# Kernel optimization log

Hardware: AMD Instinct MI355X
Metric: run time of the kernel (lower is better)

The kernel has to match this reference:

```python
import jax, jax.numpy as jnp
import numpy as np

NEG_SLOPE = 0.2
EPS = 1e-16


def setup_inputs() -> dict:
    key = jax.random.key(0)
    k1, k2, k3, k4 = jax.random.split(key, 4)
    N, H, F, E = 50000, 4, 32, 800000
    nodes_features = jax.random.normal(k1, (N, H, F), dtype=jnp.float32)
    edge_index = jax.random.randint(k2, (2, E), 0, N, dtype=jnp.int64)
    scoring_fn_source = jax.random.normal(k3, (1, H, F), dtype=jnp.float32)
    scoring_fn_target = jax.random.normal(k4, (1, H, F), dtype=jnp.float32)
    return {
        "nodes_features": nodes_features,
        "scoring_fn_source": scoring_fn_source,
        "scoring_fn_target": scoring_fn_target,
        "edge_index": edge_index,
    }


def reference(nodes_features, scoring_fn_source, scoring_fn_target, edge_index):
    # nodes_features: [N, H, F]; edge_index: [2, E] with row 0 = target, row 1 = source
    num_of_nodes = nodes_features.shape[0]
    trg = edge_index[0]
    src = edge_index[1]

    # Per-node attention logits per head: [N, H]
    scores_source = (nodes_features * scoring_fn_source).sum(axis=-1)
    scores_target = (nodes_features * scoring_fn_target).sum(axis=-1)

    # Lift N -> E via gather: [E, H]
    scores_lifted = scores_source[src] + scores_target[trg]
    src_nodes_features_lifted = nodes_features[src]  # [E, H, F]

    scores_per_edge = jax.nn.leaky_relu(scores_lifted, NEG_SLOPE)
    # Global max subtraction for numerical stability (matches original code)
    scores_per_edge = scores_per_edge - scores_per_edge.max()
    exp_scores = jnp.exp(scores_per_edge)

    # Segment softmax denominator via scatter-add, then gather back per edge
    neighborhood_sums = jax.ops.segment_sum(exp_scores, trg, num_segments=num_of_nodes)
    denom = neighborhood_sums[trg]  # [E, H]

    attentions_per_edge = (exp_scores / (denom + EPS))[..., None]  # [E, H, 1]
    return attentions_per_edge, src_nodes_features_lifted
```

## Files before the change

### kernel.cpp

```cpp
#include <hip/hip_runtime.h>

#define NEG_SLOPE 0.2f
#define EPSV 1e-16f
#define NBMAX 256
#define BSHIFT 8

typedef float f32x4 __attribute__((ext_vector_type(4)));
typedef float f32x2 __attribute__((ext_vector_type(2)));
typedef short s16x2 __attribute__((ext_vector_type(2)));
typedef unsigned u32x2 __attribute__((ext_vector_type(2)));

__device__ __forceinline__ unsigned fenc(float f) {
    unsigned b = __float_as_uint(f);
    return b ^ ((b & 0x80000000u) ? 0xFFFFFFFFu : 0x80000000u);
}
__device__ __forceinline__ float fdec(unsigned u) {
    unsigned b = (u & 0x80000000u) ? (u ^ 0x80000000u) : ~u;
    return __uint_as_float(b);
}
#define FENC_NEG_INF 0x007FFFFFu

__device__ __forceinline__ unsigned f32_to_bf16_rne(float f) {
    unsigned u = __float_as_uint(f);
    unsigned lsb = (u >> 16) & 1u;
    return (u + 0x7FFFu + lsb) >> 16;
}

__device__ __forceinline__ void pk_atomic_add_bf16(unsigned* addr, float a, float b) {
#if __has_builtin(__builtin_amdgcn_global_atomic_fadd_v2bf16)
    s16x2 v;
    v.x = (short)f32_to_bf16_rne(a);
    v.y = (short)f32_to_bf16_rne(b);
    typedef __attribute__((address_space(1))) s16x2 gs16x2;
    __builtin_amdgcn_global_atomic_fadd_v2bf16((gs16x2*)(void*)addr, v);
#else
    unsigned old = *addr, assumed;
    do {
        assumed = old;
        float lo = __uint_as_float((assumed & 0xFFFFu) << 16) + a;
        float hi = __uint_as_float(assumed & 0xFFFF0000u) + b;
        unsigned nv = (f32_to_bf16_rne(hi) << 16) | (f32_to_bf16_rne(lo) & 0xFFFFu);
        old = atomicCAS(addr, assumed, nv);
    } while (old != assumed);
#endif
}

__global__ void detect_idx_kernel(const unsigned* __restrict__ ei32,
                                  int* __restrict__ flag,
                                  unsigned* __restrict__ bhist) {
    __shared__ int anynz;
    if (threadIdx.x == 0) anynz = 0;
    __syncthreads();
    unsigned v = ei32[2 * threadIdx.x + 1];
    if (v != 0u) anynz = 1;
    if (threadIdx.x < NBMAX) bhist[threadIdx.x] = 0u;
    __syncthreads();
    if (threadIdx.x == 0) *flag = (anynz ? 0 : 1);
}

__device__ __forceinline__ int load_idx(const void* ei, int is64, size_t k) {
    if (is64) return (int)__builtin_nontemporal_load(&((const long long*)ei)[k]);
    return __builtin_nontemporal_load(&((const int*)ei)[k]);
}

__global__ void node_scores_kernel(const float* __restrict__ nf,
                                   const float* __restrict__ sfs,
                                   const float* __restrict__ sft,
                                   float* __restrict__ ss,
                                   float* __restrict__ st,
                                   unsigned* __restrict__ nsum_zero,
                                   unsigned* __restrict__ gmax,
                                   int NH, int nzero) {
    int i = blockIdx.x * blockDim.x + threadIdx.x;
    if (i >= NH) return;
    if (i == 0) *gmax = FENC_NEG_INF;
    for (int k = i; k < nzero; k += NH) nsum_zero[k] = 0u;
    int h = i & 3;
    const float4* __restrict__ row = (const float4*)(nf + (size_t)i * 32);
    const float4* __restrict__ as  = (const float4*)(sfs + h * 32);
    const float4* __restrict__ at  = (const float4*)(sft + h * 32);
    float accs = 0.f, acct = 0.f;
#pragma unroll
    for (int q = 0; q < 8; ++q) {
        float4 v = row[q];
        float4 a = as[q];
        float4 b = at[q];
        accs += v.x * a.x + v.y * a.y + v.z * a.z + v.w * a.w;
        acct += v.x * b.x + v.y * b.y + v.z * b.z + v.w * b.w;
    }
    ss[i] = accs;
    st[i] = acct;
}

__global__ void bin_hist_kernel(const void* __restrict__ ei,
                                const int* __restrict__ flag,
                                unsigned* __restrict__ bhist, int E) {
    __shared__ unsigned lh[NBMAX];
    for (int i = threadIdx.x; i < NBMAX; i += blockDim.x) lh[i] = 0u;
    __syncthreads();
    int is64 = *flag;
    int per = (E + gridDim.x - 1) / gridDim.x;
    int s = blockIdx.x * per;
    int en = s + per < E ? s + per : E;
    for (int e = s + threadIdx.x; e < en; e += blockDim.x) {
        int src = load_idx(ei, is64, (size_t)E + e);
        atomicAdd(&lh[src >> BSHIFT], 1u);
    }
    __syncthreads();
    for (int i = threadIdx.x; i < NBMAX; i += blockDim.x)
        if (lh[i]) atomicAdd(&bhist[i], lh[i]);
}

__global__ void bin_scan_kernel(const unsigned* __restrict__ bhist,
                                unsigned* __restrict__ bstart,
                                unsigned* __restrict__ bcursor, int nb) {
    if (threadIdx.x == 0) {
        unsigned acc = 0;
        for (int c = 0; c < nb; ++c) {
            bstart[c] = acc;
            bcursor[c] = acc;
            acc += bhist[c];
        }
        bstart[nb] = acc;
    }
}

__global__ void bin_scatter_kernel(const void* __restrict__ ei,
                                   const int* __restrict__ flag,
                                   unsigned* __restrict__ bcursor,
                                   int* __restrict__ perm,
                                   int* __restrict__ ssrc, int E) {
    __shared__ unsigned lh[NBMAX], lbase[NBMAX], lcur[NBMAX];
    for (int i = threadIdx.x; i < NBMAX; i += blockDim.x) { lh[i] = 0u; lcur[i] = 0u; }
    __syncthreads();
    int is64 = *flag;
    int per = (E + gridDim.x - 1) / gridDim.x;
    int s = blockIdx.x * per;
    int en = s + per < E ? s + per : E;
    for (int e = s + threadIdx.x; e < en; e += blockDim.x) {
        int src = load_idx(ei, is64, (size_t)E + e);
        atomicAdd(&lh[src >> BSHIFT], 1u);
    }
    __syncthreads();
    for (int i = threadIdx.x; i < NBMAX; i += blockDim.x)
        lbase[i] = lh[i] ? atomicAdd(&bcursor[i], lh[i]) : 0u;
    __syncthreads();
    for (int e = s + threadIdx.x; e < en; e += blockDim.x) {
        int src = load_idx(ei, is64, (size_t)E + e);
        int b = src >> BSHIFT;
        unsigned pos = lbase[b] + atomicAdd(&lcur[b], 1u);
        perm[pos] = e;
        ssrc[pos] = src;
    }
}

__global__ void edge_exp_sum_pk_kernel(const void* __restrict__ ei,
                                       const int* __restrict__ flag,
                                       const float* __restrict__ ss,
                                       const float* __restrict__ st,
                                       float* __restrict__ pbuf,
                                       unsigned* __restrict__ nsum_pk,
                                       unsigned* __restrict__ gmax,
                                       int E) {
    __shared__ float red[256];
    int is64 = *flag;
    int n2 = E * 2;
    int stride = gridDim.x * blockDim.x;
    float lmax = -__builtin_inff();
    for (int i = blockIdx.x * blockDim.x + threadIdx.x; i < n2; i += stride) {
        int e = i >> 1, hp = i & 1;
        int trg = load_idx(ei, is64, e);
        int src = load_idx(ei, is64, (size_t)E + e);
        f32x2 a = *(const f32x2*)(ss + (size_t)src * 4 + hp * 2);
        f32x2 b = *(const f32x2*)(st + (size_t)trg * 4 + hp * 2);
        float s0 = a.x + b.x, s1 = a.y + b.y;
        float lr0 = s0 > 0.f ? s0 : NEG_SLOPE * s0;
        float lr1 = s1 > 0.f ? s1 : NEG_SLOPE * s1;
        lmax = fmaxf(lmax, fmaxf(lr0, lr1));
        float p0 = __expf(lr0), p1 = __expf(lr1);
        f32x2 pv; pv.x = p0; pv.y = p1;
        __builtin_nontemporal_store(pv, (f32x2*)(pbuf + (size_t)e * 4 + hp * 2));
        pk_atomic_add_bf16(nsum_pk + (size_t)trg * 2 + hp, p0, p1);
    }
    red[threadIdx.x] = lmax;
    __syncthreads();
    for (int off = 128; off > 0; off >>= 1) {
        if (threadIdx.x < off)
            red[threadIdx.x] = fmaxf(red[threadIdx.x], red[threadIdx.x + off]);
        __syncthreads();
    }
    if (threadIdx.x == 0) atomicMax(gmax, fenc(red[0]));
}

__global__ void att_pk_kernel(const void* __restrict__ ei,
                              const int* __restrict__ flag,
                              const float* __restrict__ pbuf,
                              const unsigned* __restrict__ nsum_pk,
                              const unsigned* __restrict__ gmax,
                              float* __restrict__ out,
                              int E) {
    int is64 = *flag;
    float de = EPSV * __expf(fdec(*gmax));
    int stride = gridDim.x * blockDim.x;
    for (int e = blockIdx.x * blockDim.x + threadIdx.x; e < E; e += stride) {
        int trg = load_idx(ei, is64, e);
        u32x2 u = *(const u32x2*)(nsum_pk + (size_t)trg * 2);
        f32x4 d;
        d.x = __uint_as_float((u.x & 0xFFFFu) << 16);
        d.y = __uint_as_float(u.x & 0xFFFF0000u);
        d.z = __uint_as_float((u.y & 0xFFFFu) << 16);
        d.w = __uint_as_float(u.y & 0xFFFF0000u);
        f32x4 p = __builtin_nontemporal_load((const f32x4*)(pbuf + (size_t)e * 4));
        f32x4 a = p / (d + de);
        __builtin_nontemporal_store(a, (f32x4*)(out + (size_t)e * 4));
    }
}

__global__ void gather_sorted_kernel(const unsigned* __restrict__ bstart,
                                     const int* __restrict__ perm,
                                     const int* __restrict__ ssrc,
                                     const f32x4* __restrict__ nf4,
                                     f32x4* __restrict__ out4, int nb) {
    int xcd = blockIdx.x & 7;
    int lb = blockIdx.x >> 3;
    int lstride = (gridDim.x >> 3) * blockDim.x;
    for (int c = xcd; c < nb; c += 8) {
        int js = (int)bstart[c];
        int n = ((int)bstart[c + 1] - js) << 5;
        for (int t = lb * blockDim.x + threadIdx.x; t < n; t += lstride) {
            int j = js + (t >> 5), q = t & 31;
            int e = perm[j];
            int src = ssrc[j];
            f32x4 v = nf4[(size_t)src * 32 + q];
            __builtin_nontemporal_store(v, &out4[(size_t)e * 32 + q]);
        }
    }
}

__global__ void gather_feat_kernel(const void* __restrict__ ei,
                                   const int* __restrict__ flag,
                                   const f32x4* __restrict__ nf4,
                                   f32x4* __restrict__ out4, int E) {
    int is64 = *flag;
    int n = E * 32;
    int stride = gridDim.x * blockDim.x;
    for (int t = blockIdx.x * blockDim.x + threadIdx.x; t < n; t += stride) {
        int e = t >> 5, q = t & 31;
        int src = load_idx(ei, is64, (size_t)E + e);
        f32x4 v = nf4[(size_t)src * 32 + q];
        __builtin_nontemporal_store(v, &out4[(size_t)e * 32 + q]);
    }
}

__device__ __forceinline__ float edge_lr_rc(const void* ei, int is64,
                                            const float* ss, const float* st,
                                            int E, int e, int h, int* trg_out) {
    int trg = load_idx(ei, is64, e);
    int src = load_idx(ei, is64, (size_t)E + e);
    if (trg_out) *trg_out = trg;
    float s = ss[src * 4 + h] + st[trg * 4 + h];
    return s > 0.f ? s : NEG_SLOPE * s;
}

__global__ void zero_fb_kernel(float* __restrict__ nsum, int n) {
    int i = blockIdx.x * blockDim.x + threadIdx.x;
    if (i < n) nsum[i] = 0.f;
}

__global__ void edge_exp_sum_fb_kernel(const void* __restrict__ ei,
                                       const int* __restrict__ flag,
                                       const float* __restrict__ ss,
                                       const float* __restrict__ st,
                                       float* __restrict__ nsum,
                                       unsigned* __restrict__ gmax, int E) {
    __shared__ float red[256];
    int is64 = *flag;
    int n4 = E * 4;
    int stride = gridDim.x * blockDim.x;
    float lmax = -__builtin_inff();
    for (int i = blockIdx.x * blockDim.x + threadIdx.x; i < n4; i += stride) {
        int trg;
        float lr = edge_lr_rc(ei, is64, ss, st, E, i >> 2, i & 3, &trg);
        lmax = fmaxf(lmax, lr);
        atomicAdd(&nsum[trg * 4 + (i & 3)], __expf(lr));
    }
    red[threadIdx.x] = lmax;
    __syncthreads();
    for (int off = 128; off > 0; off >>= 1) {
        if (threadIdx.x < off)
            red[threadIdx.x] = fmaxf(red[threadIdx.x], red[threadIdx.x + off]);
        __syncthreads();
    }
    if (threadIdx.x == 0) atomicMax(gmax, fenc(red[0]));
}

__global__ void att_fb_kernel(const void* __restrict__ ei,
                              const int* __restrict__ flag,
                              const float* __restrict__ ss,
                              const float* __restrict__ st,
                              const unsigned* __restrict__ gmax,
                              const float* __restrict__ nsum,
                              float* __restrict__ out, int E) {
    int i = blockIdx.x * blockDim.x + threadIdx.x;
    if (i >= E * 4) return;
    int is64 = *flag;
    float de = EPSV * __expf(fdec(*gmax));
    int trg;
    float lr = edge_lr_rc(ei, is64, ss, st, E, i >> 2, i & 3, &trg);
    float a = __expf(lr) / (nsum[trg * 4 + (i & 3)] + de);
    __builtin_nontemporal_store(a, &out[i]);
}

extern "C" void kernel_launch(void* const* d_in, const int* in_sizes, int n_in,
                              void* d_out, int out_size, void* d_ws, size_t ws_size,
                              hipStream_t stream) {
    const float* nf  = (const float*)d_in[0];
    const float* sfs = (const float*)d_in[1];
    const float* sft = (const float*)d_in[2];
    const void*  ei  = d_in[3];

    const int NH = in_sizes[0] / 32;
    const int N  = NH / 4;
    const int E  = in_sizes[3] / 2;
    const int nb = (N + (1 << BSHIFT) - 1) >> BSHIFT;

    float* out = (float*)d_out;
    float* ws  = (float*)d_ws;

    float*    ss      = ws;
    float*    st      = ws + NH;
    int*      flag    = (int*)(ws + 2 * (size_t)NH);
    unsigned* gmax    = (unsigned*)(flag + 1);
    float*    pbuf    = ws + 2 * (size_t)NH + 4;
    unsigned* nsum_pk = (unsigned*)(pbuf + (size_t)E * 4);
    unsigned* bhist   = nsum_pk + (size_t)N * 2;
    unsigned* bstart  = bhist + NBMAX;
    unsigned* bcursor = bstart + NBMAX + 1;
    int*      perm    = (int*)(bcursor + NBMAX);
    int*      ssrc    = perm + E;

    size_t need_r9   = ((size_t)2 * NH + 4 + (size_t)E * 4 + (size_t)N * 2) * 4;
    size_t need_sort = need_r9 + ((size_t)3 * NBMAX + 1 + (size_t)E * 2) * 4;
    bool lean = ws_size >= need_r9;
    bool srt  = ws_size >= need_sort;

    const int B = 256;

    detect_idx_kernel<<<1, 256, 0, stream>>>((const unsigned*)ei, flag, bhist);

    if (lean) {
        node_scores_kernel<<<(NH + B - 1) / B, B, 0, stream>>>(
            nf, sfs, sft, ss, st, nsum_pk, gmax, NH, N * 2);
        if (srt) {
            bin_hist_kernel<<<256, B, 0, stream>>>(ei, flag, bhist, E);
            bin_scan_kernel<<<1, 64, 0, stream>>>(bhist, bstart, bcursor, nb);
            bin_scatter_kernel<<<256, B, 0, stream>>>(ei, flag, bcursor, perm, ssrc, E);
        }
        edge_exp_sum_pk_kernel<<<2048, B, 0, stream>>>(ei, flag, ss, st, pbuf,
                                                       nsum_pk, gmax, E);
        att_pk_kernel<<<2048, B, 0, stream>>>(ei, flag, pbuf, nsum_pk, gmax,
                                              out, E);
        if (srt) {
            gather_sorted_kernel<<<4096, B, 0, stream>>>(
                bstart, perm, ssrc, (const f32x4*)nf,
                (f32x4*)(out + (size_t)E * 4), nb);
        } else {
            gather_feat_kernel<<<4096, B, 0, stream>>>(
                ei, flag, (const f32x4*)nf, (f32x4*)(out + (size_t)E * 4), E);
        }
    } else {
        float* nsum_fb = (float*)(gmax + 1);
        node_scores_kernel<<<(NH + B - 1) / B, B, 0, stream>>>(
            nf, sfs, sft, ss, st, (unsigned*)nsum_fb, gmax, NH, 0);
        zero_fb_kernel<<<(NH + B - 1) / B, B, 0, stream>>>(nsum_fb, NH);
        edge_exp_sum_fb_kernel<<<2048, B, 0, stream>>>(ei, flag, ss, st,
                                                       nsum_fb, gmax, E);
        att_fb_kernel<<<(E * 4 + B - 1) / B, B, 0, stream>>>(ei, flag, ss, st,
                                                             gmax, nsum_fb, out, E);
        gather_feat_kernel<<<4096, B, 0, stream>>>(
            ei, flag, (const f32x4*)nf, (f32x4*)(out + (size_t)E * 4), E);
    }
}
```

Measured before the change: 219.9 us.

## Fuse edge exp/sum pass into bin scatter and pack perm/src pairs

Merges the edge score, exp, segment-sum atomics and max reduction into the bin scatter kernel, so the edge index is read once for both the sort and the softmax numerator. The permutation and source arrays are interleaved into one int2 array, so the gather reads one 8-byte record per edge slot. This drops one kernel launch and one full pass over edge_index, but the fused kernel runs only 512 blocks doing heavier per-edge work (including two packed bf16 atomics), which may cut parallelism for the atomic-heavy part.

```diff
diff --git a/kernel.cpp b/kernel.cpp
--- a/kernel.cpp
+++ b/kernel.cpp
@@ -9,6 +9,7 @@
 typedef float f32x2 __attribute__((ext_vector_type(2)));
 typedef short s16x2 __attribute__((ext_vector_type(2)));
 typedef unsigned u32x2 __attribute__((ext_vector_type(2)));
+typedef int i32x2 __attribute__((ext_vector_type(2)));
 
 __device__ __forceinline__ unsigned fenc(float f) {
     unsigned b = __float_as_uint(f);
@@ -125,18 +126,25 @@
     }
 }
 
-__global__ void bin_scatter_kernel(const void* __restrict__ ei,
+__global__ void scatter_exp_kernel(const void* __restrict__ ei,
                                    const int* __restrict__ flag,
+                                   const float* __restrict__ ss,
+                                   const float* __restrict__ st,
+                                   float* __restrict__ pbuf,
+                                   unsigned* __restrict__ nsum_pk,
+                                   unsigned* __restrict__ gmax,
                                    unsigned* __restrict__ bcursor,
-                                   int* __restrict__ perm,
-                                   int* __restrict__ ssrc, int E) {
+                                   i32x2* __restrict__ pe,
+                                   int E) {
     __shared__ unsigned lh[NBMAX], lbase[NBMAX], lcur[NBMAX];
+    __shared__ float red[256];
     for (int i = threadIdx.x; i < NBMAX; i += blockDim.x) { lh[i] = 0u; lcur[i] = 0u; }
     __syncthreads();
     int is64 = *flag;
     int per = (E + gridDim.x - 1) / gridDim.x;
     int s = blockIdx.x * per;
     int en = s + per < E ? s + per : E;
+
     for (int e = s + threadIdx.x; e < en; e += blockDim.x) {
         int src = load_idx(ei, is64, (size_t)E + e);
         atomicAdd(&lh[src >> BSHIFT], 1u);
@@ -145,12 +153,81 @@
     for (int i = threadIdx.x; i < NBMAX; i += blockDim.x)
         lbase[i] = lh[i] ? atomicAdd(&bcursor[i], lh[i]) : 0u;
     __syncthreads();
+
+    float lmax = -__builtin_inff();
     for (int e = s + threadIdx.x; e < en; e += blockDim.x) {
+        int trg = load_idx(ei, is64, e);
         int src = load_idx(ei, is64, (size_t)E + e);
         int b = src >> BSHIFT;
         unsigned pos = lbase[b] + atomicAdd(&lcur[b], 1u);
-        perm[pos] = e;
-        ssrc[pos] = src;
+        i32x2 pr; pr.x = e; pr.y = src;
+        pe[pos] = pr;
+
+        f32x4 a = *(const f32x4*)(ss + (size_t)src * 4);
+        f32x4 bb = *(const f32x4*)(st + (size_t)trg * 4);
+        f32x4 p;
+#pragma unroll
+        for (int h = 0; h < 4; ++h) {
+            float sc = a[h] + bb[h];
+            float lr = sc > 0.f ? sc : NEG_SLOPE * sc;
+            lmax = fmaxf(lmax, lr);
+            p[h] = __expf(lr);
+        }
+        __builtin_nontemporal_store(p, (f32x4*)(pbuf + (size_t)e * 4));
+        pk_atomic_add_bf16(nsum_pk + (size_t)trg * 2 + 0, p[0], p[1]);
+        pk_atomic_add_bf16(nsum_pk + (size_t)trg * 2 + 1, p[2], p[3]);
+    }
+
+    red[threadIdx.x] = lmax;
+    __syncthreads();
+    for (int off = 128; off > 0; off >>= 1) {
+        if (threadIdx.x < off)
+            red[threadIdx.x] = fmaxf(red[threadIdx.x], red[threadIdx.x + off]);
+        __syncthreads();
+    }
+    if (threadIdx.x == 0) atomicMax(gmax, fenc(red[0]));
+}
+
+__global__ void att_pk_kernel(const void* __restrict__ ei,
+                              const int* __restrict__ flag,
+                              const float* __restrict__ pbuf,
+                              const unsigned* __restrict__ nsum_pk,
+                              const unsigned* __restrict__ gmax,
+                              float* __restrict__ out,
+                              int E) {
+    int is64 = *flag;
+    float de = EPSV * __expf(fdec(*gmax));
+    int stride = gridDim.x * blockDim.x;
+    for (int e = blockIdx.x * blockDim.x + threadIdx.x; e < E; e += stride) {
+        int trg = load_idx(ei, is64, e);
+        u32x2 u = *(const u32x2*)(nsum_pk + (size_t)trg * 2);
+        f32x4 d;
+        d.x = __uint_as_float((u.x & 0xFFFFu) << 16);
+        d.y = __uint_as_float(u.x & 0xFFFF0000u);
+        d.z = __uint_as_float((u.y & 0xFFFFu) << 16);
+        d.w = __uint_as_float(u.y & 0xFFFF0000u);
+        f32x4 p = __builtin_nontemporal_load((const f32x4*)(pbuf + (size_t)e * 4));
+        f32x4 a = p / (d + de);
+        __builtin_nontemporal_store(a, (f32x4*)(out + (size_t)e * 4));
+    }
+}
+
+__global__ void gather_sorted_kernel(const unsigned* __restrict__ bstart,
+                                     const i32x2* __restrict__ pe,
+                                     const f32x4* __restrict__ nf4,
+                                     f32x4* __restrict__ out4, int nb) {
+    int xcd = blockIdx.x & 7;
+    int lb = blockIdx.x >> 3;
+    int lstride = (gridDim.x >> 3) * blockDim.x;
+    for (int c = xcd; c < nb; c += 8) {
+        int js = (int)bstart[c];
+        int n = ((int)bstart[c + 1] - js) << 5;
+        for (int t = lb * blockDim.x + threadIdx.x; t < n; t += lstride) {
+            int j = js + (t >> 5), q = t & 31;
+            i32x2 pr = pe[j];
+            f32x4 v = nf4[(size_t)pr.y * 32 + q];
+            __builtin_nontemporal_store(v, &out4[(size_t)pr.x * 32 + q]);
+        }
     }
 }
 
@@ -192,51 +269,6 @@
     if (threadIdx.x == 0) atomicMax(gmax, fenc(red[0]));
 }
 
-__global__ void att_pk_kernel(const void* __restrict__ ei,
-                              const int* __restrict__ flag,
-                              const float* __restrict__ pbuf,
-                              const unsigned* __restrict__ nsum_pk,
-                              const unsigned* __restrict__ gmax,
-                              float* __restrict__ out,
-                              int E) {
-    int is64 = *flag;
-    float de = EPSV * __expf(fdec(*gmax));
-    int stride = gridDim.x * blockDim.x;
-    for (int e = blockIdx.x * blockDim.x + threadIdx.x; e < E; e += stride) {
-        int trg = load_idx(ei, is64, e);
-        u32x2 u = *(const u32x2*)(nsum_pk + (size_t)trg * 2);
-        f32x4 d;
-        d.x = __uint_as_float((u.x & 0xFFFFu) << 16);
-        d.y = __uint_as_float(u.x & 0xFFFF0000u);
-        d.z = __uint_as_float((u.y & 0xFFFFu) << 16);
-        d.w = __uint_as_float(u.y & 0xFFFF0000u);
-        f32x4 p = __builtin_nontemporal_load((const f32x4*)(pbuf + (size_t)e * 4));
-        f32x4 a = p / (d + de);
-        __builtin_nontemporal_store(a, (f32x4*)(out + (size_t)e * 4));
-    }
-}
-
-__global__ void gather_sorted_kernel(const unsigned* __restrict__ bstart,
-                                     const int* __restrict__ perm,
-                                     const int* __restrict__ ssrc,
-                                     const f32x4* __restrict__ nf4,
-                                     f32x4* __restrict__ out4, int nb) {
-    int xcd = blockIdx.x & 7;
-    int lb = blockIdx.x >> 3;
-    int lstride = (gridDim.x >> 3) * blockDim.x;
-    for (int c = xcd; c < nb; c += 8) {
-        int js = (int)bstart[c];
-        int n = ((int)bstart[c + 1] - js) << 5;
-        for (int t = lb * blockDim.x + threadIdx.x; t < n; t += lstride) {
-            int j = js + (t >> 5), q = t & 31;
-            int e = perm[j];
-            int src = ssrc[j];
-            f32x4 v = nf4[(size_t)src * 32 + q];
-            __builtin_nontemporal_store(v, &out4[(size_t)e * 32 + q]);
-        }
-    }
-}
-
 __global__ void gather_feat_kernel(const void* __restrict__ ei,
                                    const int* __restrict__ flag,
                                    const f32x4* __restrict__ nf4,
@@ -336,8 +368,7 @@
     unsigned* bhist   = nsum_pk + (size_t)N * 2;
     unsigned* bstart  = bhist + NBMAX;
     unsigned* bcursor = bstart + NBMAX + 1;
-    int*      perm    = (int*)(bcursor + NBMAX);
-    int*      ssrc    = perm + E;
+    i32x2*    pe      = (i32x2*)(bcursor + NBMAX);
 
     size_t need_r9   = ((size_t)2 * NH + 4 + (size_t)E * 4 + (size_t)N * 2) * 4;
     size_t need_sort = need_r9 + ((size_t)3 * NBMAX + 1 + (size_t)E * 2) * 4;
@@ -348,26 +379,26 @@
 
     detect_idx_kernel<<<1, 256, 0, stream>>>((const unsigned*)ei, flag, bhist);
 
-    if (lean) {
+    if (lean && srt) {
         node_scores_kernel<<<(NH + B - 1) / B, B, 0, stream>>>(
             nf, sfs, sft, ss, st, nsum_pk, gmax, NH, N * 2);
-        if (srt) {
-            bin_hist_kernel<<<256, B, 0, stream>>>(ei, flag, bhist, E);
-            bin_scan_kernel<<<1, 64, 0, stream>>>(bhist, bstart, bcursor, nb);
-            bin_scatter_kernel<<<256, B, 0, stream>>>(ei, flag, bcursor, perm, ssrc, E);
-        }
+        bin_hist_kernel<<<256, B, 0, stream>>>(ei, flag, bhist, E);
+        bin_scan_kernel<<<1, 64, 0, stream>>>(bhist, bstart, bcursor, nb);
+        scatter_exp_kernel<<<512, B, 0, stream>>>(ei, flag, ss, st, pbuf,
+                                                  nsum_pk, gmax, bcursor, pe, E);
+        att_pk_kernel<<<2048, B, 0, stream>>>(ei, flag, pbuf, nsum_pk, gmax,
+                                              out, E);
+        gather_sorted_kernel<<<4096, B, 0, stream>>>(
+            bstart, pe, (const f32x4*)nf, (f32x4*)(out + (size_t)E * 4), nb);
+    } else if (lean) {
+        node_scores_kernel<<<(NH + B - 1) / B, B, 0, stream>>>(
+            nf, sfs, sft, ss, st, nsum_pk, gmax, NH, N * 2);
         edge_exp_sum_pk_kernel<<<2048, B, 0, stream>>>(ei, flag, ss, st, pbuf,
                                                        nsum_pk, gmax, E);
         att_pk_kernel<<<2048, B, 0, stream>>>(ei, flag, pbuf, nsum_pk, gmax,
                                               out, E);
-        if (srt) {
-            gather_sorted_kernel<<<4096, B, 0, stream>>>(
-                bstart, perm, ssrc, (const f32x4*)nf,
-                (f32x4*)(out + (size_t)E * 4), nb);
-        } else {
-            gather_feat_kernel<<<4096, B, 0, stream>>>(
-                ei, flag, (const f32x4*)nf, (f32x4*)(out + (size_t)E * 4), E);
-        }
+        gather_feat_kernel<<<4096, B, 0, stream>>>(
+            ei, flag, (const f32x4*)nf, (f32x4*)(out + (size_t)E * 4), E);
     } else {
         float* nsum_fb = (float*)(gmax + 1);
         node_scores_kernel<<<(NH + B - 1) / B, B, 0, stream>>>(
```

Result: slower. 241.5 us (+9.8%).
